# Kernel optimization log

Hardware: AMD Instinct MI355X
Metric: run time of the kernel (lower is better)

The kernel has to match this reference:

```python
import jax, jax.numpy as jnp
import numpy as np

NUM_HEADS = 8
GROUPS = 32
EPS = 1e-5


def group_norm(x, gamma, beta):
    # x: (b, c, L)
    b, c, L = x.shape
    xg = x.reshape(b, GROUPS, c // GROUPS, L)
    mean = xg.mean(axis=(2, 3), keepdims=True)
    var = xg.var(axis=(2, 3), keepdims=True)
    xn = ((xg - mean) / jnp.sqrt(var + EPS)).reshape(b, c, L)
    return xn * gamma[None, :, None] + beta[None, :, None]


def setup_inputs() -> dict:
    key = jax.random.key(0)
    ks = jax.random.split(key, 8)
    b, c, h, w = 8, 512, 32, 32
    inner = c  # inner_channels == -1 -> channels
    x = jax.random.normal(ks[0], (b, c, h, w), dtype=jnp.float32)
    gamma = jnp.ones((c,), dtype=jnp.float32)
    beta = jnp.zeros((c,), dtype=jnp.float32)
    Wq = jax.random.normal(ks[1], (inner, c), dtype=jnp.float32) * 0.02
    bq = jnp.zeros((inner,), dtype=jnp.float32)
    Wkv = jax.random.normal(ks[2], (2 * inner, c), dtype=jnp.float32) * 0.02
    bkv = jnp.zeros((2 * inner,), dtype=jnp.float32)
    Wo = jax.random.normal(ks[3], (c, inner), dtype=jnp.float32) * 0.02
    bo = jnp.zeros((c,), dtype=jnp.float32)
    return {"x": x, "gamma": gamma, "beta": beta, "Wq": Wq, "bq": bq,
            "Wkv": Wkv, "bkv": bkv, "Wo": Wo, "bo": bo}


def reference(x, gamma, beta, Wq, bq, Wkv, bkv, Wo, bo):
    b, c = x.shape[:2]
    spatial = x.shape[2:]
    L = int(np.prod(spatial))
    inner = Wq.shape[0]
    dh = inner // NUM_HEADS
    scale = dh ** -0.5  # NOTE: applied to BOTH q and k, as in the source

    xr = x.reshape(b, c, L)
    hn = group_norm(xr, gamma, beta)          # norm(x); also serves as context

    # 1x1 Conv1d == channel matmul
    q = jnp.einsum('oc,bcl->bol', Wq, hn) + bq[None, :, None]
    kv = jnp.einsum('oc,bcl->bol', Wkv, hn) + bkv[None, :, None]
    k, v = jnp.split(kv, 2, axis=1)

    # (b, heads, dh, L)
    qh = (q * scale).reshape(b, NUM_HEADS, dh, L)
    kh = (k * scale).reshape(b, NUM_HEADS, dh, L)
    vh = v.reshape(b, NUM_HEADS, dh, L)

    dots = jnp.einsum('bhdt,bhds->bhts', qh, kh)
    attn = jax.nn.softmax(dots.astype(jnp.float32), axis=-1).astype(dots.dtype)
    out = jnp.einsum('bhts,bhds->bhdt', attn, vh)  # (b, heads, dh, L)

    out = out.reshape(b, inner, L)
    # output Linear over the channel dim
    out = jnp.einsum('oc,bcl->bol', Wo, out) + bo[None, :, None]
    return (xr + out).reshape(b, c, *spatial)
```

## Files before the change

kernel.cpp:

```cpp
#include <hip/hip_runtime.h>
#include <math.h>

#define B_ 8
#define C_ 512
#define L_ 1024
#define NH_ 8
#define DH_ 64
#define EPS 1e-5f
#define SCALE 0.125f
#define QSCALE (0.125f * 1.44269504088896f)

typedef __bf16 bf16x8 __attribute__((ext_vector_type(8)));
typedef __bf16 bf16x4 __attribute__((ext_vector_type(4)));
typedef float  f32x4  __attribute__((ext_vector_type(4)));
typedef float  f32x16 __attribute__((ext_vector_type(16)));

#define MFMA16(a, b, c) __builtin_amdgcn_mfma_f32_16x16x32_bf16((a), (b), (c), 0, 0, 0)
#define MFMA32(a, b, c) __builtin_amdgcn_mfma_f32_32x32x16_bf16((a), (b), (c), 0, 0, 0)

__device__ __forceinline__ void glds16(const __bf16* g, __bf16* l) {
    __builtin_amdgcn_global_load_lds((const __attribute__((address_space(1))) void*)(g),
                                     (__attribute__((address_space(3))) void*)(l),
                                     16, 0, 0);
}

__global__ __launch_bounds__(256)
void prep_kernel(const float* __restrict__ Wq, const float* __restrict__ Wkv,
                 const float* __restrict__ Wo, __bf16* __restrict__ dst,
                 const float* __restrict__ x, float* __restrict__ stats) {
    __shared__ float rs[256], rss[256];
    int bid = blockIdx.x, tid = threadIdx.x;
    if (bid < 1024) {
        int idx = bid * 256 + tid;
        float4 v;
        if (idx < 65536)        v = ((const float4*)Wq)[idx];
        else if (idx < 196608)  v = ((const float4*)Wkv)[idx - 65536];
        else                    v = ((const float4*)Wo)[idx - 196608];
        bf16x4 o;
        o[0] = (__bf16)v.x; o[1] = (__bf16)v.y; o[2] = (__bf16)v.z; o[3] = (__bf16)v.w;
        ((bf16x4*)dst)[idx] = o;
        return;
    }
    int bg = bid - 1024;
    size_t goff = (size_t)bg * 16 * L_;
    const float4* x4 = (const float4*)(x + goff);
    float s = 0.f, ss = 0.f;
    for (int i = tid; i < 4096; i += 256) {
        float4 v = x4[i];
        s  += v.x + v.y + v.z + v.w;
        ss += v.x * v.x + v.y * v.y + v.z * v.z + v.w * v.w;
    }
    rs[tid] = s; rss[tid] = ss;
    __syncthreads();
    for (int off = 128; off > 0; off >>= 1) {
        if (tid < off) { rs[tid] += rs[tid + off]; rss[tid] += rss[tid + off]; }
        __syncthreads();
    }
    if (tid == 0) {
        const float inv_n = 1.f / 16384.f;
        float mean = rs[0] * inv_n;
        float var  = rss[0] * inv_n - mean * mean;
        stats[bg * 2]     = mean;
        stats[bg * 2 + 1] = rsqrtf(var + EPS);
    }
}

__global__ __launch_bounds__(256)
void gn_apply_kernel(const float* __restrict__ x, const float* __restrict__ gamma,
                     const float* __restrict__ beta, const float* __restrict__ stats,
                     __bf16* __restrict__ hnT) {
    __shared__ __bf16 T[32 * 520];
    const int lt = blockIdx.x, b = blockIdx.y;
    const int tid = threadIdx.x;
    const int l0 = lt * 32;
    const int cbase = tid >> 3, fl = tid & 7;
#pragma unroll
    for (int p = 0; p < 16; ++p) {
        int cc = cbase + p * 32;
        float4 v = *(const float4*)&x[((size_t)b * C_ + cc) * L_ + l0 + fl * 4];
        int bg = b * 32 + (cc >> 4);
        float m = stats[bg * 2], rstd = stats[bg * 2 + 1];
        float ga = gamma[cc] * rstd, be = beta[cc];
        T[(fl * 4 + 0) * 520 + cc] = (__bf16)((v.x - m) * ga + be);
        T[(fl * 4 + 1) * 520 + cc] = (__bf16)((v.y - m) * ga + be);
        T[(fl * 4 + 2) * 520 + cc] = (__bf16)((v.z - m) * ga + be);
        T[(fl * 4 + 3) * 520 + cc] = (__bf16)((v.w - m) * ga + be);
    }
    __syncthreads();
    const int lrow = tid >> 6, cu = tid & 63;
#pragma unroll
    for (int pp = 0; pp < 8; ++pp) {
        int l = pp * 4 + lrow;
        bf16x8 r = *(const bf16x8*)&T[l * 520 + cu * 8];
        *(bf16x8*)&hnT[((size_t)b * L_ + l0 + l) * C_ + cu * 8] = r;
    }
}

__device__ __forceinline__
void gemm_mainloop(const __bf16* __restrict__ A, const __bf16* __restrict__ Bp,
                   __bf16* As, __bf16* Bs, f32x4 acc[4][4]) {
    const int tid = threadIdx.x;
    const int lane = tid & 63, w = tid >> 6;
    const int c = lane & 15, q = lane >> 4;
    const int wm = (w >> 1) * 64, wn = (w & 1) * 64;
    const int l8 = lane >> 3, kgsw = (lane & 7) ^ l8;

    for (int k0 = 0; k0 < 512; k0 += 64) {
#pragma unroll
        for (int i = 0; i < 4; ++i) {
            int chunk = w * 4 + i;
            int row = chunk * 8 + l8;
            glds16(A  + (size_t)row * 512 + k0 + kgsw * 8, &As[chunk * 512]);
            glds16(Bp + (size_t)row * 512 + k0 + kgsw * 8, &Bs[chunk * 512]);
        }
        __syncthreads();
#pragma unroll
        for (int ks = 0; ks < 2; ++ks) {
            const int koff = ((ks * 4 + q) ^ (c & 7)) * 8;
            bf16x8 af[4], bfr[4];
#pragma unroll
            for (int m = 0; m < 4; ++m)
                af[m] = *(const bf16x8*)&As[(wm + m * 16 + c) * 64 + koff];
#pragma unroll
            for (int n = 0; n < 4; ++n)
                bfr[n] = *(const bf16x8*)&Bs[(wn + n * 16 + c) * 64 + koff];
#pragma unroll
            for (int m = 0; m < 4; ++m)
#pragma unroll
                for (int n = 0; n < 4; ++n)
                    acc[m][n] = MFMA16(af[m], bfr[n], acc[m][n]);
        }
        __syncthreads();
    }
}

__global__ __launch_bounds__(256)
void qkv_kernel(const __bf16* __restrict__ Wq_bf, const __bf16* __restrict__ Wkv_bf,
                const __bf16* __restrict__ hnT,
                const float* __restrict__ bq, const float* __restrict__ bkv,
                __bf16* __restrict__ qT, __bf16* __restrict__ kT,
                __bf16* __restrict__ vv) {
    __shared__ __bf16 SMEM[128 * 64 * 2];
    __bf16* As = SMEM;
    __bf16* Bs = SMEM + 128 * 64;
    const int b = blockIdx.y;
    const int xx = blockIdx.x;
    const int sec = xx >> 5, t = xx & 31;
    const __bf16* hb = hnT + (size_t)b * L_ * C_;

    const __bf16 *A, *Bp;
    int m0, n0;
    if (sec < 2) {
        m0 = (t & 3) * 128; n0 = (t >> 2) * 128;
        A  = (sec == 0 ? Wq_bf : Wkv_bf) + (size_t)m0 * 512;
        Bp = hb + (size_t)n0 * 512;
    } else {
        m0 = (t >> 2) * 128; n0 = (t & 3) * 128;
        A  = hb + (size_t)m0 * 512;
        Bp = Wkv_bf + (size_t)(512 + n0) * 512;
    }

    f32x4 acc[4][4];
#pragma unroll
    for (int m = 0; m < 4; ++m)
#pragma unroll
        for (int n = 0; n < 4; ++n)
#pragma unroll
            for (int r = 0; r < 4; ++r) acc[m][n][r] = 0.f;

    gemm_mainloop(A, Bp, As, Bs, acc);

    const int tid = threadIdx.x, lane = tid & 63, w = tid >> 6;
    const int c = lane & 15, q = lane >> 4;
    const int wm = (w >> 1) * 64, wn = (w & 1) * 64;

    __bf16* T2 = SMEM;
    const float* bias = (sec == 0) ? bq : bkv;
    const float scl = (sec == 0) ? QSCALE : SCALE;
#pragma unroll
    for (int mt = 0; mt < 4; ++mt)
#pragma unroll
        for (int nt = 0; nt < 4; ++nt) {
            int n_loc = wn + nt * 16 + c;
            int u4 = (wm >> 2) + mt * 4 + q;
            int u4sw = u4 ^ ((n_loc & 7) << 1);
            bf16x4 ov;
            if (sec < 2) {
                int ob = m0 + wm + mt * 16 + q * 4;
#pragma unroll
                for (int r = 0; r < 4; ++r)
                    ov[r] = (__bf16)((acc[mt][nt][r] + bias[ob + r]) * scl);
            } else {
                float bi = bkv[512 + n0 + n_loc];
#pragma unroll
                for (int r = 0; r < 4; ++r)
                    ov[r] = (__bf16)(acc[mt][nt][r] + bi);
            }
            *(bf16x4*)&T2[n_loc * 128 + u4sw * 4] = ov;
        }
    __syncthreads();
#pragma unroll
    for (int p = 0; p < 8; ++p) {
        int rrow = p * 16 + (tid >> 4);
        int u16 = tid & 15;
        int u4p = (u16 * 2) ^ ((rrow & 7) << 1);
        bf16x8 val = *(const bf16x8*)&T2[rrow * 128 + u4p * 4];
        if (sec < 2) {
            int l = n0 + rrow;
            int og = m0 + u16 * 8;
            int hh = og >> 6, d0 = og & 63;
            __bf16* dstp = (sec == 0) ? qT : kT;
            *(bf16x8*)&dstp[((size_t)(b * NH_ + hh) * L_ + l) * DH_ + d0] = val;
        } else {
            int o = n0 + rrow;
            int lg = m0 + u16 * 8;
            *(bf16x8*)&vv[((size_t)b * C_ + o) * L_ + lg] = val;
        }
    }
}

__global__ __launch_bounds__(256, 2)
void attn_kernel(const __bf16* __restrict__ qT, const __bf16* __restrict__ kT,
                 const __bf16* __restrict__ vv, __bf16* __restrict__ aoT) {
    const int bid = blockIdx.x;
    const int wg = (bid & 7) * 64 + (bid >> 3);
    const int tt = wg & 7, h = (wg >> 3) & 7, b = wg >> 6;
    const int t0 = tt * 128;
    __shared__ __bf16 Qs[128 * 64];
    __shared__ __bf16 Ks[2][64 * 64];
    __shared__ __bf16 Vs[2][64 * 64];

    const int tid = threadIdx.x, lane = tid & 63, w = tid >> 6;
    const int l8 = lane >> 3, kg = (lane & 7) ^ l8;
    const int ln = lane & 31, hi = lane >> 5, r7 = ln & 7;

    const __bf16* qbase = qT + ((size_t)(b * NH_ + h) * L_ + t0) * DH_;
    const __bf16* kbase = kT + (size_t)(b * NH_ + h) * L_ * DH_;
    const __bf16* vbase = vv + (size_t)(b * C_ + h * DH_) * L_;

#pragma unroll
    for (int i = 0; i < 4; ++i) {
        int chunk = w * 4 + i;
        glds16(qbase + (size_t)(chunk * 8 + l8) * DH_ + kg * 8, &Qs[chunk * 512]);
    }
#pragma unroll
    for (int buf = 0; buf < 2; ++buf)
#pragma unroll
        for (int i = 0; i < 2; ++i) {
            int chunk = w * 2 + i, row = chunk * 8 + l8;
            glds16(kbase + (size_t)(buf * 64 + row) * DH_ + kg * 8, &Ks[buf][chunk * 512]);
            glds16(vbase + (size_t)row * L_ + buf * 64 + kg * 8, &Vs[buf][chunk * 512]);
        }
    asm volatile("s_waitcnt vmcnt(4)" ::: "memory");
    asm volatile("s_barrier" ::: "memory");

    f32x16 o_acc[2];
#pragma unroll
    for (int dt = 0; dt < 2; ++dt)
#pragma unroll
        for (int r = 0; r < 16; ++r) o_acc[dt][r] = 0.f;
    float l_own = 0.f;

    const int qrow = w * 32 + ln;

    for (int it = 0; it < 16; ++it) {
        const __bf16* Kc = Ks[it & 1];
        const __bf16* Vc = Vs[it & 1];

        f32x16 sres[2];
#pragma unroll
        for (int mt = 0; mt < 2; ++mt)
#pragma unroll
            for (int r = 0; r < 16; ++r) sres[mt][r] = 0.f;
#pragma unroll
        for (int ks = 0; ks < 4; ++ks) {
            bf16x8 bQ = *(const bf16x8*)&Qs[qrow * 64 + ((ks * 2 + hi) ^ r7) * 8];
#pragma unroll
            for (int mt = 0; mt < 2; ++mt) {
                bf16x8 aK = *(const bf16x8*)&Kc[(mt * 32 + ln) * 64 + ((ks * 2 + hi) ^ r7) * 8];
                sres[mt] = MFMA32(aK, bQ, sres[mt]);
            }
        }

        bf16x8 frag[4];
#pragma unroll
        for (int mt = 0; mt < 2; ++mt) {
            float pv[16];
#pragma unroll
            for (int r = 0; r < 16; ++r) pv[r] = exp2f(sres[mt][r]);
            float s0a = (pv[0] + pv[1]) + (pv[2] + pv[3]);
            float s1a = (pv[4] + pv[5]) + (pv[6] + pv[7]);
            float s2a = (pv[8] + pv[9]) + (pv[10] + pv[11]);
            float s3a = (pv[12] + pv[13]) + (pv[14] + pv[15]);
            l_own += (s0a + s1a) + (s2a + s3a);
            unsigned int P[8];
#pragma unroll
            for (int j = 0; j < 8; ++j)
                asm("v_cvt_pk_bf16_f32 %0, %1, %2" : "=v"(P[j]) : "v"(pv[2 * j]), "v"(pv[2 * j + 1]));
            asm("v_permlane32_swap_b32 %0, %1" : "+v"(P[0]), "+v"(P[2]));
            asm("v_permlane32_swap_b32 %0, %1" : "+v"(P[1]), "+v"(P[3]));
            asm("v_permlane32_swap_b32 %0, %1" : "+v"(P[4]), "+v"(P[6]));
            asm("v_permlane32_swap_b32 %0, %1" : "+v"(P[5]), "+v"(P[7]));
            union FU { unsigned int u[4]; bf16x8 v; } fa, fb;
            fa.u[0] = P[0]; fa.u[1] = P[1]; fa.u[2] = P[2]; fa.u[3] = P[3];
            fb.u[0] = P[4]; fb.u[1] = P[5]; fb.u[2] = P[6]; fb.u[3] = P[7];
            frag[mt * 2 + 0] = fa.v;
            frag[mt * 2 + 1] = fb.v;
        }

#pragma unroll
        for (int ks2 = 0; ks2 < 4; ++ks2) {
#pragma unroll
            for (int dt = 0; dt < 2; ++dt) {
                bf16x8 aV = *(const bf16x8*)&Vc[(dt * 32 + ln) * 64 + ((ks2 * 2 + hi) ^ r7) * 8];
                o_acc[dt] = MFMA32(aV, frag[ks2], o_acc[dt]);
            }
        }

        asm volatile("s_barrier" ::: "memory");
        if (it < 14) {
            int s0n = (it + 2) * 64;
#pragma unroll
            for (int i = 0; i < 2; ++i) {
                int chunk = w * 2 + i, row = chunk * 8 + l8;
                glds16(kbase + (size_t)(s0n + row) * DH_ + kg * 8, &Ks[it & 1][chunk * 512]);
                glds16(vbase + (size_t)row * L_ + s0n + kg * 8, &Vs[it & 1][chunk * 512]);
            }
            asm volatile("s_waitcnt vmcnt(4)" ::: "memory");
        } else {
            asm volatile("s_waitcnt vmcnt(0)" ::: "memory");
        }
        asm volatile("s_barrier" ::: "memory");
    }

    float l_tot = l_own + __shfl_xor(l_own, 32);
    float linv = 1.f / l_tot;
    const int tg = t0 + w * 32 + ln;
    __bf16* aobase = aoT + ((size_t)b * L_ + tg) * C_ + h * DH_;
#pragma unroll
    for (int dt = 0; dt < 2; ++dt)
#pragma unroll
        for (int rq = 0; rq < 4; ++rq) {
            bf16x4 ov;
#pragma unroll
            for (int j = 0; j < 4; ++j) ov[j] = (__bf16)(o_acc[dt][rq * 4 + j] * linv);
            *(bf16x4*)&aobase[dt * 32 + rq * 8 + hi * 4] = ov;
        }
}

__global__ __launch_bounds__(256)
void proj_kernel(const __bf16* __restrict__ aoT, const __bf16* __restrict__ Wo_bf,
                 const float* __restrict__ bo, const float* __restrict__ x,
                 float* __restrict__ out) {
    __shared__ __bf16 As[128 * 64], Bs[128 * 64];
    const int b = blockIdx.y, t = blockIdx.x;
    const int m0 = (t >> 2) * 128;
    const int n0 = (t & 3) * 128;
    const __bf16* A  = aoT + (size_t)b * L_ * C_ + (size_t)m0 * 512;
    const __bf16* Bp = Wo_bf + (size_t)n0 * 512;

    f32x4 acc[4][4];
#pragma unroll
    for (int m = 0; m < 4; ++m)
#pragma unroll
        for (int n = 0; n < 4; ++n)
#pragma unroll
            for (int r = 0; r < 4; ++r) acc[m][n][r] = 0.f;

    gemm_mainloop(A, Bp, As, Bs, acc);

    const int tid = threadIdx.x, lane = tid & 63, w = tid >> 6;
    const int c = lane & 15, q = lane >> 4;
    const int wm = (w >> 1) * 64, wn = (w & 1) * 64;

#pragma unroll
    for (int mt = 0; mt < 4; ++mt)
#pragma unroll
        for (int nt = 0; nt < 4; ++nt) {
            int lb = m0 + wm + mt * 16 + q * 4;
            int o  = n0 + wn + nt * 16 + c;
            float bi = bo[o];
            size_t off = ((size_t)b * C_ + o) * L_ + lb;
            float4 xv = *(const float4*)&x[off];
            float4 rv;
            rv.x = acc[mt][nt][0] + bi + xv.x;
            rv.y = acc[mt][nt][1] + bi + xv.y;
            rv.z = acc[mt][nt][2] + bi + xv.z;
            rv.w = acc[mt][nt][3] + bi + xv.w;
            *(float4*)&out[off] = rv;
        }
}

extern "C" void kernel_launch(void* const* d_in, const int* in_sizes, int n_in,
                              void* d_out, int out_size, void* d_ws, size_t ws_size,
                              hipStream_t stream) {
    const float* x     = (const float*)d_in[0];
    const float* gamma = (const float*)d_in[1];
    const float* beta  = (const float*)d_in[2];
    const float* Wq    = (const float*)d_in[3];
    const float* bq    = (const float*)d_in[4];
    const float* Wkv   = (const float*)d_in[5];
    const float* bkv   = (const float*)d_in[6];
    const float* Wo    = (const float*)d_in[7];
    const float* bo    = (const float*)d_in[8];
    float* out = (float*)d_out;

    __bf16* wsb = (__bf16*)d_ws;
    __bf16* Wq_bf  = wsb;
    __bf16* Wkv_bf = wsb + 262144;
    __bf16* Wo_bf  = wsb + 786432;
    __bf16* hnT    = wsb + 1048576;
    __bf16* qT     = wsb + 5242880;
    __bf16* kT     = wsb + 9437184;
    __bf16* vv     = wsb + 13631488;
    __bf16* aoT    = wsb + 17825792;
    float*  stats  = (float*)(wsb + 22020096);

    prep_kernel<<<dim3(1280), 256, 0, stream>>>(Wq, Wkv, Wo, wsb, x, stats);
    gn_apply_kernel<<<dim3(32, B_), 256, 0, stream>>>(x, gamma, beta, stats, hnT);
    qkv_kernel<<<dim3(96, B_), 256, 0, stream>>>(Wq_bf, Wkv_bf, hnT, bq, bkv, qT, kT, vv);
    attn_kernel<<<dim3(512), 256, 0, stream>>>(qT, kT, vv, aoT);
    proj_kernel<<<dim3(32, B_), 256, 0, stream>>>(aoT, Wo_bf, bo, x, out);
}
```

Measured before the change: 166.5 us.

## Keep Q in registers, compute row sums via MFMA, remap blocks for XCD locality

Result: slower. 172.5 us (+3.6%).

```diff
diff --git a/kernel.cpp b/kernel.cpp
--- a/kernel.cpp
+++ b/kernel.cpp
@@ -143,8 +143,10 @@
     __shared__ __bf16 SMEM[128 * 64 * 2];
     __bf16* As = SMEM;
     __bf16* Bs = SMEM + 128 * 64;
-    const int b = blockIdx.y;
-    const int xx = blockIdx.x;
+    const int bid = blockIdx.x;
+    const int wgid = (bid & 7) * 96 + (bid >> 3);
+    const int b = wgid / 96;
+    const int xx = wgid % 96;
     const int sec = xx >> 5, t = xx & 31;
     const __bf16* hb = hnT + (size_t)b * L_ * C_;
 
@@ -219,14 +221,13 @@
     }
 }
 
-__global__ __launch_bounds__(256, 2)
+__global__ __launch_bounds__(256, 3)
 void attn_kernel(const __bf16* __restrict__ qT, const __bf16* __restrict__ kT,
                  const __bf16* __restrict__ vv, __bf16* __restrict__ aoT) {
     const int bid = blockIdx.x;
     const int wg = (bid & 7) * 64 + (bid >> 3);
     const int tt = wg & 7, h = (wg >> 3) & 7, b = wg >> 6;
     const int t0 = tt * 128;
-    __shared__ __bf16 Qs[128 * 64];
     __shared__ __bf16 Ks[2][64 * 64];
     __shared__ __bf16 Vs[2][64 * 64];
 
@@ -238,11 +239,12 @@
     const __bf16* kbase = kT + (size_t)(b * NH_ + h) * L_ * DH_;
     const __bf16* vbase = vv + (size_t)(b * C_ + h * DH_) * L_;
 
-#pragma unroll
-    for (int i = 0; i < 4; ++i) {
-        int chunk = w * 4 + i;
-        glds16(qbase + (size_t)(chunk * 8 + l8) * DH_ + kg * 8, &Qs[chunk * 512]);
-    }
+    const int qrow = w * 32 + ln;
+    bf16x8 qf[4];
+#pragma unroll
+    for (int ks = 0; ks < 4; ++ks)
+        qf[ks] = *(const bf16x8*)&qbase[(size_t)qrow * DH_ + (ks * 2 + hi) * 8];
+
 #pragma unroll
     for (int buf = 0; buf < 2; ++buf)
 #pragma unroll
@@ -254,33 +256,40 @@
     asm volatile("s_waitcnt vmcnt(4)" ::: "memory");
     asm volatile("s_barrier" ::: "memory");
 
-    f32x16 o_acc[2];
+    bf16x8 aOnes;
+    {
+        __bf16 one = (__bf16)((ln == 0) ? 1.f : 0.f);
+#pragma unroll
+        for (int j = 0; j < 8; ++j) aOnes[j] = one;
+    }
+
+    f32x16 o_acc[2], o_l;
 #pragma unroll
     for (int dt = 0; dt < 2; ++dt)
 #pragma unroll
         for (int r = 0; r < 16; ++r) o_acc[dt][r] = 0.f;
-    float l_own = 0.f;
-
-    const int qrow = w * 32 + ln;
+#pragma unroll
+    for (int r = 0; r < 16; ++r) o_l[r] = 0.f;
 
     for (int it = 0; it < 16; ++it) {
-        const __bf16* Kc = Ks[it & 1];
-        const __bf16* Vc = Vs[it & 1];
+        const __bf16* Kc = &Ks[it & 1][0];
+        const __bf16* Vc = &Vs[it & 1][0];
 
         f32x16 sres[2];
 #pragma unroll
         for (int mt = 0; mt < 2; ++mt)
 #pragma unroll
             for (int r = 0; r < 16; ++r) sres[mt][r] = 0.f;
+        __builtin_amdgcn_s_setprio(1);
 #pragma unroll
         for (int ks = 0; ks < 4; ++ks) {
-            bf16x8 bQ = *(const bf16x8*)&Qs[qrow * 64 + ((ks * 2 + hi) ^ r7) * 8];
 #pragma unroll
             for (int mt = 0; mt < 2; ++mt) {
                 bf16x8 aK = *(const bf16x8*)&Kc[(mt * 32 + ln) * 64 + ((ks * 2 + hi) ^ r7) * 8];
-                sres[mt] = MFMA32(aK, bQ, sres[mt]);
+                sres[mt] = MFMA32(aK, qf[ks], sres[mt]);
             }
         }
+        __builtin_amdgcn_s_setprio(0);
 
         bf16x8 frag[4];
 #pragma unroll
@@ -288,11 +297,6 @@
             float pv[16];
 #pragma unroll
             for (int r = 0; r < 16; ++r) pv[r] = exp2f(sres[mt][r]);
-            float s0a = (pv[0] + pv[1]) + (pv[2] + pv[3]);
-            float s1a = (pv[4] + pv[5]) + (pv[6] + pv[7]);
-            float s2a = (pv[8] + pv[9]) + (pv[10] + pv[11]);
-            float s3a = (pv[12] + pv[13]) + (pv[14] + pv[15]);
-            l_own += (s0a + s1a) + (s2a + s3a);
             unsigned int P[8];
 #pragma unroll
             for (int j = 0; j < 8; ++j)
@@ -308,6 +312,7 @@
             frag[mt * 2 + 1] = fb.v;
         }
 
+        __builtin_amdgcn_s_setprio(1);
 #pragma unroll
         for (int ks2 = 0; ks2 < 4; ++ks2) {
 #pragma unroll
@@ -315,16 +320,20 @@
                 bf16x8 aV = *(const bf16x8*)&Vc[(dt * 32 + ln) * 64 + ((ks2 * 2 + hi) ^ r7) * 8];
                 o_acc[dt] = MFMA32(aV, frag[ks2], o_acc[dt]);
             }
-        }
+            o_l = MFMA32(aOnes, frag[ks2], o_l);
+        }
+        __builtin_amdgcn_s_setprio(0);
 
         asm volatile("s_barrier" ::: "memory");
         if (it < 14) {
             int s0n = (it + 2) * 64;
+            __bf16* Kw = &Ks[it & 1][0];
+            __bf16* Vw = &Vs[it & 1][0];
 #pragma unroll
             for (int i = 0; i < 2; ++i) {
                 int chunk = w * 2 + i, row = chunk * 8 + l8;
-                glds16(kbase + (size_t)(s0n + row) * DH_ + kg * 8, &Ks[it & 1][chunk * 512]);
-                glds16(vbase + (size_t)row * L_ + s0n + kg * 8, &Vs[it & 1][chunk * 512]);
+                glds16(kbase + (size_t)(s0n + row) * DH_ + kg * 8, &Kw[chunk * 512]);
+                glds16(vbase + (size_t)row * L_ + s0n + kg * 8, &Vw[chunk * 512]);
             }
             asm volatile("s_waitcnt vmcnt(4)" ::: "memory");
         } else {
@@ -333,8 +342,8 @@
         asm volatile("s_barrier" ::: "memory");
     }
 
-    float l_tot = l_own + __shfl_xor(l_own, 32);
-    float linv = 1.f / l_tot;
+    float lsum = __shfl(o_l[0], ln);
+    float linv = 1.f / lsum;
     const int tg = t0 + w * 32 + ln;
     __bf16* aobase = aoT + ((size_t)b * L_ + tg) * C_ + h * DH_;
 #pragma unroll
@@ -353,7 +362,9 @@
                  const float* __restrict__ bo, const float* __restrict__ x,
                  float* __restrict__ out) {
     __shared__ __bf16 As[128 * 64], Bs[128 * 64];
-    const int b = blockIdx.y, t = blockIdx.x;
+    const int bid = blockIdx.x;
+    const int wgid = (bid & 7) * 32 + (bid >> 3);
+    const int b = wgid >> 5, t = wgid & 31;
     const int m0 = (t >> 2) * 128;
     const int n0 = (t & 3) * 128;
     const __bf16* A  = aoT + (size_t)b * L_ * C_ + (size_t)m0 * 512;
@@ -418,7 +429,7 @@
 
     prep_kernel<<<dim3(1280), 256, 0, stream>>>(Wq, Wkv, Wo, wsb, x, stats);
     gn_apply_kernel<<<dim3(32, B_), 256, 0, stream>>>(x, gamma, beta, stats, hnT);
-    qkv_kernel<<<dim3(96, B_), 256, 0, stream>>>(Wq_bf, Wkv_bf, hnT, bq, bkv, qT, kT, vv);
+    qkv_kernel<<<dim3(768), 256, 0, stream>>>(Wq_bf, Wkv_bf, hnT, bq, bkv, qT, kT, vv);
     attn_kernel<<<dim3(512), 256, 0, stream>>>(qT, kT, vv, aoT);
-    proj_kernel<<<dim3(32, B_), 256, 0, stream>>>(aoT, Wo_bf, bo, x, out);
-}
+    proj_kernel<<<dim3(256), 256, 0, stream>>>(aoT, Wo_bf, bo, x, out);
+}
```
